# Kernel tuning notes

Hardware: AMD Instinct MI355X
Metric: run time of the kernel (lower is better)

## Reference

```python
import jax, jax.numpy as jnp
import numpy as np


def _maxpool2(x):
    # 2x2 max pool, stride 2, on NCHW
    b, c, h, w = x.shape
    return x.reshape(b, c, h // 2, 2, w // 2, 2).max(axis=(3, 5))


def _conv1x1(w, x):
    # w: [out_c, in_c], x: [B, in_c, H, W]
    return jnp.einsum('oc,bchw->bohw', w, x)


def setup_inputs() -> dict:
    key = jax.random.key(0)
    ks = jax.random.split(key, 5)
    B, C, H, W = 16, 64, 64, 64
    x = jax.random.normal(ks[0], (B, C, H, W), dtype=jnp.float32)
    # 1x1 conv weights (spectral-norm treated as already-normalized params)
    Wt = jax.random.normal(ks[1], (C // 8, C), dtype=jnp.float32) * 0.05
    Wp = jax.random.normal(ks[2], (C // 8, C), dtype=jnp.float32) * 0.05
    Wg = jax.random.normal(ks[3], (C // 2, C), dtype=jnp.float32) * 0.05
    Wo = jax.random.normal(ks[4], (C, C // 2), dtype=jnp.float32) * 0.05
    gamma = jnp.float32(0.5)  # nonzero so attention branch contributes
    return {"x": x, "Wt": Wt, "Wp": Wp, "Wg": Wg, "Wo": Wo, "gamma": gamma}


def reference(x, Wt, Wp, Wg, Wo, gamma):
    b, c, h, w = x.shape
    theta = _conv1x1(Wt, x).reshape(b, c // 8, h * w)            # [B, C/8, HW]
    phi = _maxpool2(_conv1x1(Wp, x)).reshape(b, c // 8, -1)      # [B, C/8, HW/4]
    g = _maxpool2(_conv1x1(Wg, x)).reshape(b, c // 2, -1)        # [B, C/2, HW/4]
    # scores: [B, HW, HW/4]; softmax over pooled (key) axis
    beta = jax.nn.softmax(jnp.einsum('bct,bcs->bts', theta, phi), axis=-1)
    o = jnp.einsum('bcs,bts->bct', g, beta).reshape(b, c // 2, h, w)
    o = _conv1x1(Wo, o)                                          # [B, C, H, W]
    return gamma * o + x
```

## Files before the change

kernel.cpp:

```cpp
#include <hip/hip_runtime.h>
#include <math.h>

#define NB   16
#define NC   64
#define HWs  4096
#define NPS  1024
#define LOG2E 1.44269504088896341f

static constexpr size_t PHI_OFF = (size_t)NB * HWs * 8;
static constexpr size_t GT_OFF  = PHI_OFF + (size_t)NB * NPS * 8;

typedef short s16x8 __attribute__((ext_vector_type(8)));
typedef float f32x4 __attribute__((ext_vector_type(4)));

#define LD8G(p) (*(const s16x8*)(p))
#define SB()    __builtin_amdgcn_sched_barrier(0)

__device__ inline unsigned short f2bf(float f) {
    unsigned int u = __float_as_uint(f);
    u += 0x7fffu + ((u >> 16) & 1u);
    return (unsigned short)(u >> 16);
}
__device__ inline unsigned int pk2(float a, float b) {
    unsigned int ua = __float_as_uint(a); ua += 0x7fffu + ((ua >> 16) & 1u);
    unsigned int ub = __float_as_uint(b); ub += 0x7fffu + ((ub >> 16) & 1u);
    return (ua >> 16) | (ub & 0xffff0000u);
}

__global__ __launch_bounds__(256) __attribute__((amdgpu_waves_per_eu(4, 4)))
void k_proj(
    const float* __restrict__ x, const float* __restrict__ Wt,
    const float* __restrict__ Wp, const float* __restrict__ Wg,
    unsigned short* __restrict__ ws)
{
    __shared__ float xs[64 * 128];

    unsigned short* theta = ws;
    unsigned short* phi   = ws + PHI_OFF;
    unsigned short* gT    = ws + GT_OFF;

    const int tid  = threadIdx.x;
    const int blk  = blockIdx.x;
    const int b    = blk >> 6;
    const int rp   = (blk >> 1) & 31;
    const int half = blk & 1;

    const float* xsrc = x + (size_t)b * NC * HWs + rp * 128;
#pragma unroll
    for (int i = 0; i < 8; ++i) {
        const int idx = i * 256 + tid;
        const int ci  = idx >> 5;
        const int f4  = idx & 31;
        float4 v = *(const float4*)(xsrc + (size_t)ci * HWs + f4 * 4);
        *(float4*)(xs + ci * 128 + f4 * 4) = v;
    }
    __syncthreads();

    const int h   = tid & 127;
    const int sub = __builtin_amdgcn_readfirstlane(tid >> 7);
    const int row = h & 1;
    const int col = h >> 1;
    const int px  = row * 64 + col;

    float a4[4], ag8[8];
#pragma unroll
    for (int j = 0; j < 4; ++j) a4[j] = 0.f;
#pragma unroll
    for (int j = 0; j < 8; ++j) ag8[j] = 0.f;

    const float* W8 = (half ? Wp : Wt) + sub * 4 * NC;
    const float* WG = Wg + (half * 16 + sub * 8) * NC;

#pragma unroll 4
    for (int ci = 0; ci < NC; ++ci) {
        const float xv = xs[ci * 128 + px];
#pragma unroll
        for (int j = 0; j < 4; ++j) a4[j] += W8[j * NC + ci] * xv;
#pragma unroll
        for (int j = 0; j < 8; ++j) ag8[j] += WG[j * NC + ci] * xv;
    }

    if (half == 0) {
        const int q = (2 * rp + row) * 64 + col;
        uint2 pkd;
        pkd.x = pk2(a4[0] * LOG2E, a4[1] * LOG2E);
        pkd.y = pk2(a4[2] * LOG2E, a4[3] * LOG2E);
        *(uint2*)(theta + ((size_t)b * HWs + q) * 8 + sub * 4) = pkd;
    } else {
#pragma unroll
        for (int j = 0; j < 4; ++j) {
            float v = a4[j];
            v = fmaxf(v, __shfl_xor(v, 1));
            v = fmaxf(v, __shfl_xor(v, 2));
            a4[j] = v;
        }
    }

#pragma unroll
    for (int j = 0; j < 8; ++j) {
        float v = ag8[j];
        v = fmaxf(v, __shfl_xor(v, 1));
        v = fmaxf(v, __shfl_xor(v, 2));
        ag8[j] = v;
    }

    if ((h & 3) == 0) {
        const int ps = rp * 32 + (h >> 2);
        if (half == 1) {
            uint2 pkd;
            pkd.x = pk2(a4[0], a4[1]);
            pkd.y = pk2(a4[2], a4[3]);
            *(uint2*)(phi + ((size_t)b * NPS + ps) * 8 + sub * 4) = pkd;
        }
#pragma unroll
        for (int j = 0; j < 8; ++j) {
            const int c = half * 16 + sub * 8 + j;
            gT[((size_t)b * 32 + c) * NPS + ps] = f2bf(ag8[j]);
        }
    }
}

__global__ __launch_bounds__(256) __attribute__((amdgpu_waves_per_eu(4, 4)))
void k_attn(
    const float* __restrict__ x, const float* __restrict__ Wo,
    const float* __restrict__ gamma_p, const unsigned short* __restrict__ ws,
    float* __restrict__ out)
{
    __shared__ __align__(16) unsigned char smem[26624];

    const int tid  = threadIdx.x;
    const int wave = __builtin_amdgcn_readfirstlane(tid >> 6);
    const int lane = tid & 63;
    const int quad = lane >> 4, lr = lane & 15;
    const int blk  = blockIdx.x;
    const int b    = blk >> 6;
    const int q0   = (blk & 63) * 64;
    const int stoff = blk & 15;

    const unsigned short* th = ws + (size_t)b * HWs * 8;
    const unsigned short* ph = ws + PHI_OFF + (size_t)b * NPS * 8;
    const unsigned short* gp = ws + GT_OFF + (size_t)b * 32 * NPS;
    unsigned short* Pw  = (unsigned short*)smem + wave * 2304;
    unsigned short* stg = (unsigned short*)(smem + 18432);

    const int sch   = tid >> 3;
    const int spart = tid & 7;
    const int swz   = spart ^ (sch & 7);
    const int voff_gc = sch * (NPS * 2) + spart * 16;

    const s16x8 zf = {0, 0, 0, 0, 0, 0, 0, 0};
    const f32x4 zc = {0.f, 0.f, 0.f, 0.f};

    const s16x8 thA = (quad == 0) ? LD8G(th + (size_t)(q0 + wave * 16 + lr) * 8) : zf;

    f32x4 O[2];
    f32x4 l4;
#pragma unroll
    for (int r = 0; r < 4; ++r) { O[0][r] = 0.f; O[1][r] = 0.f; l4[r] = 0.f; }

    const int voff_ph0 = (0 * 16 + lr) * 16;
    const int voff_ph1 = (1 * 16 + lr) * 16;
    const int voff_ph2 = (2 * 16 + lr) * 16;
    const int voff_ph3 = (3 * 16 + lr) * 16;

    s16x8 phB_e[4], phB_o[4];
    s16x8 greg_e, greg_o;

#define GL4(dst, off, base)                                                   \
    asm volatile("global_load_dwordx4 %0, %1, %2"                             \
                 : "=v"(dst) : "v"(off), "s"(base) : "memory")

#define LOADPH_A(dst, baseT)                                                  \
    GL4(dst[0], voff_ph0, baseT); GL4(dst[1], voff_ph1, baseT);               \
    GL4(dst[2], voff_ph2, baseT); GL4(dst[3], voff_ph3, baseT);

#define WAITVM(n) asm volatile("s_waitcnt vmcnt(" #n ")" ::: "memory")

#define QK(Sv, phB)                                                           \
    _Pragma("unroll")                                                         \
    for (int ss = 0; ss < 4; ++ss)                                            \
        Sv[ss] = __builtin_amdgcn_mfma_f32_16x16x32_bf16(thA, phB[ss], zc, 0, 0, 0);

#define EXPST(Sv, wbuf)                                                       \
    _Pragma("unroll")                                                         \
    for (int ss = 0; ss < 4; ++ss)                                            \
        _Pragma("unroll")                                                     \
        for (int r = 0; r < 4; ++r) {                                         \
            const float p = exp2f(Sv[ss][r]);                                 \
            l4[r] += p;                                                       \
            Pw[(wbuf) + (quad * 4 + r) * 72 + ss * 16 + lr] =                 \
                (unsigned short)(__float_as_uint(p) >> 16);                   \
        }

#define BODY(phCUR, phNXT, gCUR, gNXT, curT, LAST)                            \
    {                                                                         \
        WAITVM(4);              \
        __syncthreads();                                                      \
        *(s16x8*)(stg + ((curT) & 1) * 2048 + sch * 64 + swz * 8) = gCUR;     \
        if (!(LAST)) {                                                        \
            const int stn = ((curT) + 1 + stoff) & 15;                        \
            GL4(gNXT, voff_gc, gp + (size_t)stn * 64);                        \
            LOADPH_A(phNXT, ph + (size_t)stn * 512);                          \
        }                                                                     \
        const int pb = ((curT) - 1) & 1;                                      \
        const s16x8 Pf0 = *(const s16x8*)(Pw + pb * 1152 + lr * 72 + quad * 8);      \
        const s16x8 Pf1 = *(const s16x8*)(Pw + pb * 1152 + lr * 72 + 32 + quad * 8); \
        s16x8 Gf[2][2];                                                       \
        _Pragma("unroll")                                                     \
        for (int kc = 0; kc < 2; ++kc)                                        \
            _Pragma("unroll")                                                 \
            for (int cs = 0; cs < 2; ++cs)                                    \
                Gf[kc][cs] = *(const s16x8*)(stg + pb * 2048 +                \
                    (cs * 16 + lr) * 64 + ((kc * 4 + quad) ^ (lr & 7)) * 8);  \
        if (LAST) { WAITVM(0); } else { WAITVM(5); }       \
        SB();                                                                 \
        f32x4 S[4];                                                           \
        QK(S, phCUR);                                                         \
        _Pragma("unroll")                                                     \
        for (int cs = 0; cs < 2; ++cs)                                        \
            O[cs] = __builtin_amdgcn_mfma_f32_16x16x32_bf16(Pf0, Gf[0][cs], O[cs], 0, 0, 0); \
        _Pragma("unroll")                                                     \
        for (int cs = 0; cs < 2; ++cs)                                        \
            O[cs] = __builtin_amdgcn_mfma_f32_16x16x32_bf16(Pf1, Gf[1][cs], O[cs], 0, 0, 0); \
        EXPST(S, ((curT) & 1) * 1152);                                        \
    }

    {
        const int st0 = stoff;
        const int st1 = (stoff + 1) & 15;
        GL4(greg_e, voff_gc, gp + (size_t)st0 * 64);
        LOADPH_A(phB_e, ph + (size_t)st0 * 512);
        WAITVM(4);
        *(s16x8*)(stg + 0 * 2048 + sch * 64 + swz * 8) = greg_e;
        GL4(greg_o, voff_gc, gp + (size_t)st1 * 64);
        LOADPH_A(phB_o, ph + (size_t)st1 * 512);
        WAITVM(5);
        SB();
        f32x4 S[4];
        QK(S, phB_e);
        EXPST(S, 0);
    }

    for (int t = 1; t < 15; t += 2) {
        BODY(phB_o, phB_e, greg_o, greg_e, t,     0);
        BODY(phB_e, phB_o, greg_e, greg_o, t + 1, 0);
    }
    BODY(phB_o, phB_e, greg_o, greg_e, 15, 1);

    {
        __syncthreads();
        const s16x8 Pf0 = *(const s16x8*)(Pw + 1152 + lr * 72 + quad * 8);
        const s16x8 Pf1 = *(const s16x8*)(Pw + 1152 + lr * 72 + 32 + quad * 8);
        s16x8 Gf[2][2];
#pragma unroll
        for (int kc = 0; kc < 2; ++kc)
#pragma unroll
            for (int cs = 0; cs < 2; ++cs)
                Gf[kc][cs] = *(const s16x8*)(stg + 2048 +
                    (cs * 16 + lr) * 64 + ((kc * 4 + quad) ^ (lr & 7)) * 8);
#pragma unroll
        for (int cs = 0; cs < 2; ++cs)
            O[cs] = __builtin_amdgcn_mfma_f32_16x16x32_bf16(Pf0, Gf[0][cs], O[cs], 0, 0, 0);
#pragma unroll
        for (int cs = 0; cs < 2; ++cs)
            O[cs] = __builtin_amdgcn_mfma_f32_16x16x32_bf16(Pf1, Gf[1][cs], O[cs], 0, 0, 0);
    }

#pragma unroll
    for (int r = 0; r < 4; ++r) {
        float v = l4[r];
        v += __shfl_xor(v, 1);
        v += __shfl_xor(v, 2);
        v += __shfl_xor(v, 4);
        v += __shfl_xor(v, 8);
        l4[r] = 1.f / v;
    }

    __syncthreads();
    float* otile = (float*)smem;
#pragma unroll
    for (int cs = 0; cs < 2; ++cs) {
        f32x4 v;
#pragma unroll
        for (int r = 0; r < 4; ++r) v[r] = O[cs][r] * l4[r];
        *(f32x4*)(otile + (cs * 16 + lr) * 68 + wave * 16 + quad * 4) = v;
    }
    __syncthreads();

    const int qq = tid & 63;
    const int quarter = __builtin_amdgcn_readfirstlane(tid >> 6);
    float ov[32];
#pragma unroll
    for (int c = 0; c < 32; ++c) ov[c] = otile[c * 68 + qq];
    const float gam = gamma_p[0];
#pragma unroll
    for (int j = 0; j < 16; ++j) {
        const float* wrow = Wo + (size_t)(quarter * 16 + j) * 32;
        float a = 0.f;
#pragma unroll
        for (int c = 0; c < 32; ++c) a += wrow[c] * ov[c];
        const size_t ad = ((size_t)b * NC + quarter * 16 + j) * HWs + q0 + qq;
        out[ad] = gam * a + x[ad];
    }
}

extern "C" void kernel_launch(void* const* d_in, const int* in_sizes, int n_in,
                              void* d_out, int out_size, void* d_ws, size_t ws_size,
                              hipStream_t stream) {
    const float* x     = (const float*)d_in[0];
    const float* Wt    = (const float*)d_in[1];
    const float* Wp    = (const float*)d_in[2];
    const float* Wg    = (const float*)d_in[3];
    const float* Wo    = (const float*)d_in[4];
    const float* gamma = (const float*)d_in[5];
    float* out = (float*)d_out;
    unsigned short* ws = (unsigned short*)d_ws;

    k_proj<<<1024, 256, 0, stream>>>(x, Wt, Wp, Wg, ws);
    k_attn<<<1024, 256, 0, stream>>>(x, Wo, gamma, ws, out);
}
```

Before: 114.2 us.

## Split projection kernel into 2048 blocks with fewer channels per thread

The projection kernel now gives each block a half-width column slab (32 columns across two rows) and spreads output channels over four waves, so each thread accumulates 2+4 channels instead of 4+8. The grid doubles to 2048 blocks, LDS per block halves, and the waves-per-EU hint rises to 8, aiming at higher occupancy and more parallelism in this memory-bound prologue. The pooling shuffle pattern changes to match the new pixel mapping (xor 32 for the row pair, xor 1 for the column pair). In exchange, each block issues narrower global stores, and weight loads are repeated across more blocks.

```diff
diff --git a/kernel.cpp b/kernel.cpp
--- a/kernel.cpp
+++ b/kernel.cpp
@@ -27,13 +27,13 @@
     return (ua >> 16) | (ub & 0xffff0000u);
 }
 
-__global__ __launch_bounds__(256) __attribute__((amdgpu_waves_per_eu(4, 4)))
+__global__ __launch_bounds__(256) __attribute__((amdgpu_waves_per_eu(8, 8)))
 void k_proj(
     const float* __restrict__ x, const float* __restrict__ Wt,
     const float* __restrict__ Wp, const float* __restrict__ Wg,
     unsigned short* __restrict__ ws)
 {
-    __shared__ float xs[64 * 128];
+    __shared__ float xs[64 * 64];
 
     unsigned short* theta = ws;
     unsigned short* phi   = ws + PHI_OFF;
@@ -41,81 +41,80 @@
 
     const int tid  = threadIdx.x;
     const int blk  = blockIdx.x;
-    const int b    = blk >> 6;
-    const int rp   = (blk >> 1) & 31;
-    const int half = blk & 1;
+    const int b    = blk >> 7;
+    const int rp   = (blk >> 2) & 31;
+    const int half = (blk >> 1) & 1;
+    const int csub = blk & 1;
+    const int col0 = csub * 32;
 
     const float* xsrc = x + (size_t)b * NC * HWs + rp * 128;
 #pragma unroll
-    for (int i = 0; i < 8; ++i) {
-        const int idx = i * 256 + tid;
-        const int ci  = idx >> 5;
-        const int f4  = idx & 31;
-        float4 v = *(const float4*)(xsrc + (size_t)ci * HWs + f4 * 4);
-        *(float4*)(xs + ci * 128 + f4 * 4) = v;
+    for (int i = 0; i < 4; ++i) {
+        const int idx  = i * 256 + tid;
+        const int ci   = idx >> 4;
+        const int slot = idx & 15;
+        const int r    = slot >> 3;
+        const int c4   = slot & 7;
+        float4 v = *(const float4*)(xsrc + (size_t)ci * HWs + r * 64 + col0 + c4 * 4);
+        *(float4*)(xs + ci * 64 + r * 32 + c4 * 4) = v;
     }
     __syncthreads();
 
-    const int h   = tid & 127;
-    const int sub = __builtin_amdgcn_readfirstlane(tid >> 7);
-    const int row = h & 1;
-    const int col = h >> 1;
-    const int px  = row * 64 + col;
-
-    float a4[4], ag8[8];
-#pragma unroll
-    for (int j = 0; j < 4; ++j) a4[j] = 0.f;
-#pragma unroll
-    for (int j = 0; j < 8; ++j) ag8[j] = 0.f;
-
-    const float* W8 = (half ? Wp : Wt) + sub * 4 * NC;
-    const float* WG = Wg + (half * 16 + sub * 8) * NC;
-
-#pragma unroll 4
+    const int pxl = tid & 63;
+    const int r   = pxl >> 5;
+    const int c   = pxl & 31;
+    const int grp = __builtin_amdgcn_readfirstlane(tid >> 6);
+
+    float a2[2], ag4[4];
+#pragma unroll
+    for (int j = 0; j < 2; ++j) a2[j] = 0.f;
+#pragma unroll
+    for (int j = 0; j < 4; ++j) ag4[j] = 0.f;
+
+    const float* W8 = (half ? Wp : Wt) + grp * 2 * NC;
+    const float* WG = Wg + (half * 16 + grp * 4) * NC;
+
+#pragma unroll 8
     for (int ci = 0; ci < NC; ++ci) {
-        const float xv = xs[ci * 128 + px];
-#pragma unroll
-        for (int j = 0; j < 4; ++j) a4[j] += W8[j * NC + ci] * xv;
-#pragma unroll
-        for (int j = 0; j < 8; ++j) ag8[j] += WG[j * NC + ci] * xv;
+        const float xv = xs[ci * 64 + pxl];
+#pragma unroll
+        for (int j = 0; j < 2; ++j) a2[j] += W8[j * NC + ci] * xv;
+#pragma unroll
+        for (int j = 0; j < 4; ++j) ag4[j] += WG[j * NC + ci] * xv;
     }
 
     if (half == 0) {
-        const int q = (2 * rp + row) * 64 + col;
-        uint2 pkd;
-        pkd.x = pk2(a4[0] * LOG2E, a4[1] * LOG2E);
-        pkd.y = pk2(a4[2] * LOG2E, a4[3] * LOG2E);
-        *(uint2*)(theta + ((size_t)b * HWs + q) * 8 + sub * 4) = pkd;
+        const int q = (2 * rp + r) * 64 + col0 + c;
+        *(unsigned int*)(theta + ((size_t)b * HWs + q) * 8 + grp * 2) =
+            pk2(a2[0] * LOG2E, a2[1] * LOG2E);
     } else {
 #pragma unroll
+        for (int j = 0; j < 2; ++j) {
+            float v = a2[j];
+            v = fmaxf(v, __shfl_xor(v, 32));
+            v = fmaxf(v, __shfl_xor(v, 1));
+            a2[j] = v;
+        }
+    }
+
+#pragma unroll
+    for (int j = 0; j < 4; ++j) {
+        float v = ag4[j];
+        v = fmaxf(v, __shfl_xor(v, 32));
+        v = fmaxf(v, __shfl_xor(v, 1));
+        ag4[j] = v;
+    }
+
+    if (r == 0 && (c & 1) == 0) {
+        const int ps = rp * 32 + csub * 16 + (c >> 1);
+        if (half == 1) {
+            *(unsigned int*)(phi + ((size_t)b * NPS + ps) * 8 + grp * 2) =
+                pk2(a2[0], a2[1]);
+        }
+#pragma unroll
         for (int j = 0; j < 4; ++j) {
-            float v = a4[j];
-            v = fmaxf(v, __shfl_xor(v, 1));
-            v = fmaxf(v, __shfl_xor(v, 2));
-            a4[j] = v;
-        }
-    }
-
-#pragma unroll
-    for (int j = 0; j < 8; ++j) {
-        float v = ag8[j];
-        v = fmaxf(v, __shfl_xor(v, 1));
-        v = fmaxf(v, __shfl_xor(v, 2));
-        ag8[j] = v;
-    }
-
-    if ((h & 3) == 0) {
-        const int ps = rp * 32 + (h >> 2);
-        if (half == 1) {
-            uint2 pkd;
-            pkd.x = pk2(a4[0], a4[1]);
-            pkd.y = pk2(a4[2], a4[3]);
-            *(uint2*)(phi + ((size_t)b * NPS + ps) * 8 + sub * 4) = pkd;
-        }
-#pragma unroll
-        for (int j = 0; j < 8; ++j) {
-            const int c = half * 16 + sub * 8 + j;
-            gT[((size_t)b * 32 + c) * NPS + ps] = f2bf(ag8[j]);
+            const int ch = half * 16 + grp * 4 + j;
+            gT[((size_t)b * 32 + ch) * NPS + ps] = f2bf(ag4[j]);
         }
     }
 }
@@ -316,6 +315,6 @@
     float* out = (float*)d_out;
     unsigned short* ws = (unsigned short*)d_ws;
 
-    k_proj<<<1024, 256, 0, stream>>>(x, Wt, Wp, Wg, ws);
+    k_proj<<<2048, 256, 0, stream>>>(x, Wt, Wp, Wg, ws);
     k_attn<<<1024, 256, 0, stream>>>(x, Wo, gamma, ws, out);
 }
```

New measurement: 112.0 us. 1.02x faster.
